# Performance work log

Hardware: AMD Instinct MI355X
Metric: run time of the kernel (lower is better)

Reference implementation:

```python
import jax, jax.numpy as jnp
import numpy as np

N_ROUTES = 512
N_TIMES = 4096
N_MOVES = 16384
N_NODES = 2048
N_CDF = 8192
ALPHA, BETA = 0.15, 4


def setup_inputs() -> dict:
    key = jax.random.key(0)
    ks = jax.random.split(key, 7)
    x_raw = jax.random.normal(ks[0], (N_ROUTES, N_TIMES), dtype=jnp.float32)
    A = (jax.random.uniform(ks[1], (N_MOVES, N_ROUTES)) < 0.05).astype(jnp.float32)
    movement_node = jax.random.randint(ks[2], (N_MOVES,), 0, N_NODES, dtype=jnp.int32)
    cdf_node = jax.random.randint(ks[3], (N_CDF,), 0, N_NODES, dtype=jnp.int32)
    t_free = jax.random.uniform(ks[4], (N_CDF,), minval=0.5, maxval=2.0, dtype=jnp.float32)
    cap = jax.random.uniform(ks[5], (N_CDF,), minval=100.0, maxval=1000.0, dtype=jnp.float32)
    radio = jax.random.uniform(ks[6], (N_CDF,), minval=0.5, maxval=1.5, dtype=jnp.float32)
    return {
        "x_raw": x_raw, "A": A,
        "t_free": t_free, "cap": cap, "radio": radio,
        "movement_node": movement_node, "cdf_node": cdf_node,
        "n_nodes": N_NODES,
    }


def reference(x_raw, A, t_free, cap, radio, movement_node, cdf_node, n_nodes):
    # x = relu(param).clamp(min=0) -> relu is sufficient
    x = jax.nn.relu(x_raw)                                  # [R, T]
    c_pred = A @ x                                          # [M, T]
    # per-node flow: sum of all movement rows sharing the same node
    node_flow = jax.ops.segment_sum(c_pred, movement_node, num_segments=n_nodes)  # [N, T]
    flow = node_flow[cdf_node]                              # [C, T]
    # BPR congestion delay per c_df row
    ratio = jnp.clip(flow / cap[:, None], 1e-6)
    delay_cong = t_free[:, None] * ALPHA * radio[:, None] * ratio ** BETA
    y_rows = t_free[:, None] * radio[:, None] + delay_cong  # [C, T]
    y_l_t_hat = y_rows.sum(axis=0)                          # [T]
    return x, c_pred, y_l_t_hat
```

## Files before the change

### kernel.cpp

```cpp
#include <hip/hip_runtime.h>

#define N_ROUTES 512
#define N_TIMES  4096
#define N_MOVES  16384
#define N_NODES  2048
#define N_CDF    8192
#define ALPHA    0.15f
#define NODE_CAP 32

typedef unsigned short ushort_t;
typedef __attribute__((ext_vector_type(8))) short short8;
typedef __attribute__((ext_vector_type(4))) float floatx4;


__device__ inline ushort_t f2bf(float f) {
    union { float f; unsigned u; } v; v.f = f;
    unsigned r = (v.u + 0x7FFFu + ((v.u >> 16) & 1u)) >> 16;
    return (ushort_t)r;
}

__global__ __launch_bounds__(256) void transpose_bf(const float* __restrict__ xr,
                                                    float* __restrict__ xo,
                                                    ushort_t* __restrict__ xT) {
    __shared__ float ld[64][65];
    int t0 = blockIdx.x * 64;
    int k0 = blockIdx.y * 64;
    int tid = threadIdx.x;
    int col = tid & 63;
    #pragma unroll
    for (int i = 0; i < 16; ++i) {
        int row = i * 4 + (tid >> 6);
        float v = fmaxf(xr[(size_t)(k0 + row) * N_TIMES + t0 + col], 0.f);
        ld[row][col] = v;
        xo[(size_t)(k0 + row) * N_TIMES + t0 + col] = v;
    }
    __syncthreads();
    int trow = tid >> 2;
    int kgrp = (tid & 3) * 16;
    ushort_t __align__(16) tmp[16];
    #pragma unroll
    for (int j = 0; j < 16; ++j) tmp[j] = f2bf(ld[kgrp + j][trow]);
    ushort_t* dst = xT + (size_t)(t0 + trow) * 512 + k0 + kgrp;
    *(uint4*)dst       = ((uint4*)tmp)[0];
    *(uint4*)(dst + 8) = ((uint4*)tmp)[1];
}

__global__ __launch_bounds__(256) void convA(const float* __restrict__ A,
                                             ushort_t* __restrict__ Ab) {
    size_t i = (size_t)(blockIdx.x * 256 + threadIdx.x) * 8;
    const float4* s = (const float4*)(A + i);
    float4 a = s[0], b = s[1];
    ushort_t __align__(16) t[8] = {f2bf(a.x), f2bf(a.y), f2bf(a.z), f2bf(a.w),
                                   f2bf(b.x), f2bf(b.y), f2bf(b.z), f2bf(b.w)};
    *(uint4*)(Ab + i) = *(uint4*)t;
}

__global__ __launch_bounds__(256) void build_nodes(const int* __restrict__ mnode,
                                                   int* __restrict__ ncnt,
                                                   int* __restrict__ nlist) {
    int m = blockIdx.x * blockDim.x + threadIdx.x;
    if (m >= N_MOVES) return;
    int n = mnode[m];
    int slot = atomicAdd(&ncnt[n], 1);
    if (slot < NODE_CAP) nlist[(size_t)n * NODE_CAP + slot] = m;
}

__global__ __launch_bounds__(128) void sa_kernel(const float* __restrict__ A,
                                                 const int* __restrict__ ncnt,
                                                 const int* __restrict__ nlist,
                                                 ushort_t* __restrict__ SAb) {
    int n = blockIdx.x, tid = threadIdx.x;
    int cnt = min(ncnt[n], NODE_CAP);
    float acc0 = 0.f, acc1 = 0.f, acc2 = 0.f, acc3 = 0.f;
    for (int j = 0; j < cnt; ++j) {
        int m = nlist[(size_t)n * NODE_CAP + j];
        float4 v = *(const float4*)(A + (size_t)m * 512 + tid * 4);
        acc0 += v.x; acc1 += v.y; acc2 += v.z; acc3 += v.w;
    }
    ushort_t __align__(8) t[4] = {f2bf(acc0), f2bf(acc1), f2bf(acc2), f2bf(acc3)};
    *(uint2*)(SAb + (size_t)n * 512 + tid * 4) = *(uint2*)t;
}

__global__ __launch_bounds__(256) void wsum_kernel(const float* __restrict__ t_free,
                                                   const float* __restrict__ cap,
                                                   const float* __restrict__ radio,
                                                   const int* __restrict__ cdf_node,
                                                   float* __restrict__ w,
                                                   float* __restrict__ basep) {
    int c = blockIdx.x * 256 + threadIdx.x;
    float tr = t_free[c] * radio[c];
    float ic = 1.0f / cap[c];
    float ic2 = ic * ic;
    atomicAdd(&w[cdf_node[c]], ALPHA * tr * ic2 * ic2);
    float b = tr;
    #pragma unroll
    for (int d = 32; d >= 1; d >>= 1) b += __shfl_down(b, d);
    if ((threadIdx.x & 63) == 0) atomicAdd(basep, b);
}

__global__ __launch_bounds__(256) void y_init(const float* __restrict__ basep,
                                              float* __restrict__ y) {
    y[blockIdx.x * 256 + threadIdx.x] = *basep;
}

#define GLOAD_LDS16(g, l) __builtin_amdgcn_global_load_lds( \
    (const __attribute__((address_space(1))) void*)(g),     \
    (__attribute__((address_space(3))) void*)(l), 16, 0, 0)

__global__ __launch_bounds__(256) void gemm_fused(const ushort_t* __restrict__ Abig,
                                                  const ushort_t* __restrict__ Bbf,
                                                  float* __restrict__ c_pred,
                                                  const float* __restrict__ w,
                                                  float* __restrict__ y) {
    __shared__ __align__(16) ushort_t Atile[2][128 * 64];
    __shared__ __align__(16) ushort_t Btile[2][128 * 64];

    const int tid  = threadIdx.x;
    const int wv   = tid >> 6;
    const int lane = tid & 63;
    const int quad = lane >> 4;
    const int l16  = lane & 15;
    const int bn   = blockIdx.x;
    const int bm   = blockIdx.y;

    const int mi = (wv & 1) * 64;
    const int ni = (wv >> 1) * 64;

    floatx4 acc[4][4] = {};

    const int srow = lane >> 3;
    const int schk = lane & 7;

    const ushort_t* gA = Abig + (size_t)(bm * 128) * 512;
    const ushort_t* gB = Bbf  + (size_t)(bn * 128) * 512;

#define STAGE(buf, kt)                                                       \
    {                                                                        \
        _Pragma("unroll")                                                    \
        for (int c = 0; c < 4; ++c) {                                        \
            int rowbase = wv * 32 + c * 8;                                   \
            int row = rowbase + srow;                                        \
            int cl  = schk ^ (row & 7);                                      \
            GLOAD_LDS16(gA + (size_t)row * 512 + (kt) * 64 + cl * 8,         \
                        &Atile[buf][rowbase * 64]);                          \
            GLOAD_LDS16(gB + (size_t)row * 512 + (kt) * 64 + cl * 8,         \
                        &Btile[buf][rowbase * 64]);                          \
        }                                                                    \
    }

    STAGE(0, 0);
    __syncthreads();

    int cur = 0;
    #pragma unroll
    for (int kt = 0; kt < 8; ++kt) {
        if (kt < 7) STAGE(cur ^ 1, kt + 1);

        #pragma unroll
        for (int kk = 0; kk < 2; ++kk) {
            short8 af[4], bf[4];
            #pragma unroll
            for (int fi = 0; fi < 4; ++fi) {
                int row = mi + fi * 16 + l16;
                int cp  = (kk * 4 + quad) ^ (row & 7);
                af[fi] = *(const short8*)(&Atile[cur][row * 64 + cp * 8]);
            }
            #pragma unroll
            for (int fj = 0; fj < 4; ++fj) {
                int row = ni + fj * 16 + l16;
                int cp  = (kk * 4 + quad) ^ (row & 7);
                bf[fj] = *(const short8*)(&Btile[cur][row * 64 + cp * 8]);
            }
            #pragma unroll
            for (int fi = 0; fi < 4; ++fi)
                #pragma unroll
                for (int fj = 0; fj < 4; ++fj)
                    acc[fi][fj] = __builtin_amdgcn_mfma_f32_16x16x32_bf16(
                        af[fi], bf[fj], acc[fi][fj], 0, 0, 0);
        }

        if (kt < 7) {
            __syncthreads();
            cur ^= 1;
        }
    }
#undef STAGE

    if (bm < 128) {
        #pragma unroll
        for (int fi = 0; fi < 4; ++fi) {
            #pragma unroll
            for (int reg = 0; reg < 4; ++reg) {
                size_t row = (size_t)bm * 128 + mi + fi * 16 + quad * 4 + reg;
                float* cp = c_pred + row * N_TIMES + bn * 128 + ni + l16;
                #pragma unroll
                for (int fj = 0; fj < 4; ++fj)
                    cp[fj * 16] = acc[fi][fj][reg];
            }
        }
    } else {
        int nb = (bm - 128) * 128;
        float psum[4] = {0.f, 0.f, 0.f, 0.f};
        #pragma unroll
        for (int fj = 0; fj < 4; ++fj)
            #pragma unroll
            for (int fi = 0; fi < 4; ++fi)
                #pragma unroll
                for (int reg = 0; reg < 4; ++reg) {
                    int n = nb + mi + fi * 16 + quad * 4 + reg;
                    float f = acc[fi][fj][reg];
                    float f2 = f * f;
                    psum[fj] += w[n] * f2 * f2;
                }
        #pragma unroll
        for (int fj = 0; fj < 4; ++fj) {
            float v = psum[fj];
            v += __shfl_xor(v, 16);
            v += __shfl_xor(v, 32);
            if (quad == 0)
                atomicAdd(&y[bn * 128 + ni + fj * 16 + l16], v);
        }
    }
}

extern "C" void kernel_launch(void* const* d_in, const int* in_sizes, int n_in,
                              void* d_out, int out_size, void* d_ws, size_t ws_size,
                              hipStream_t stream) {
    const float* x_raw         = (const float*)d_in[0];
    const float* A             = (const float*)d_in[1];
    const float* t_free        = (const float*)d_in[2];
    const float* cap           = (const float*)d_in[3];
    const float* radio         = (const float*)d_in[4];
    const int*   movement_node = (const int*)d_in[5];
    const int*   cdf_node      = (const int*)d_in[6];

    float* out    = (float*)d_out;
    float* x_out  = out;
    float* c_pred = out + (size_t)N_ROUTES * N_TIMES;
    float* y      = c_pred + (size_t)N_MOVES * N_TIMES;

    char* ws = (char*)d_ws;
    ushort_t* Abig  = (ushort_t*)(ws);
    ushort_t* SAb   = Abig + (size_t)N_MOVES * 512;
    ushort_t* xTbf  = (ushort_t*)(ws + 18874368);
    int*      ncnt  = (int*)(ws + 23068672);
    int*      nlist = (int*)(ws + 23076864);
    float*    w     = (float*)(ws + 23339008);
    float*    basep = (float*)(ws + 23347200);

    hipMemsetAsync(ncnt, 0, N_NODES * sizeof(int), stream);
    hipMemsetAsync(w, 0, N_NODES * sizeof(float), stream);
    hipMemsetAsync(basep, 0, sizeof(float), stream);

    transpose_bf<<<dim3(N_TIMES / 64, N_ROUTES / 64), dim3(256), 0, stream>>>(
        x_raw, x_out, xTbf);

    convA<<<dim3((int)((size_t)N_MOVES * 512 / 8 / 256)), dim3(256), 0, stream>>>(A, Abig);

    build_nodes<<<dim3(N_MOVES / 256), dim3(256), 0, stream>>>(movement_node, ncnt, nlist);

    sa_kernel<<<dim3(N_NODES), dim3(128), 0, stream>>>(A, ncnt, nlist, SAb);

    wsum_kernel<<<dim3(N_CDF / 256), dim3(256), 0, stream>>>(
        t_free, cap, radio, cdf_node, w, basep);

    y_init<<<dim3(N_TIMES / 256), dim3(256), 0, stream>>>(basep, y);

    gemm_fused<<<dim3(N_TIMES / 128, (N_MOVES + N_NODES) / 128), dim3(256), 0, stream>>>(
        Abig, xTbf, c_pred, w, y);
}
```

Before: 412.9 us.

## Restructure fused GEMM into 256x256 tiles with 8-wave ping-pong pipeline

Moves the fused GEMM from 128x128 tiles and 4 waves to 256x256 tiles and 8 waves. It splits each K-step into quadrant MFMA phases that interleave LDS reads, async global-to-LDS loads with explicit vmcnt waits and raw s_barrier, and uses s_setprio around the MFMA bursts. A 1D grid with an XCD-aware swizzle replaces the 2D grid. The goal is more data reuse per tile and better overlap of memory with matrix cores. The cost is higher register and LDS pressure (128KB LDS per block) and hand-tuned barrier ordering that is fragile.

```diff
diff --git a/kernel.cpp b/kernel.cpp
--- a/kernel.cpp
+++ b/kernel.cpp
@@ -107,107 +107,153 @@
     (const __attribute__((address_space(1))) void*)(g),     \
     (__attribute__((address_space(3))) void*)(l), 16, 0, 0)
 
-__global__ __launch_bounds__(256) void gemm_fused(const ushort_t* __restrict__ Abig,
-                                                  const ushort_t* __restrict__ Bbf,
-                                                  float* __restrict__ c_pred,
-                                                  const float* __restrict__ w,
-                                                  float* __restrict__ y) {
-    __shared__ __align__(16) ushort_t Atile[2][128 * 64];
-    __shared__ __align__(16) ushort_t Btile[2][128 * 64];
+__global__ __launch_bounds__(512, 2) void gemm_fused(const ushort_t* __restrict__ Abig,
+                                                     const ushort_t* __restrict__ Bbf,
+                                                     float* __restrict__ c_pred,
+                                                     const float* __restrict__ w,
+                                                     float* __restrict__ y) {
+    __shared__ __align__(16) ushort_t lds[4][256 * 64];
 
     const int tid  = threadIdx.x;
     const int wv   = tid >> 6;
     const int lane = tid & 63;
     const int quad = lane >> 4;
     const int l16  = lane & 15;
-    const int bn   = blockIdx.x;
-    const int bm   = blockIdx.y;
-
-    const int mi = (wv & 1) * 64;
-    const int ni = (wv >> 1) * 64;
-
-    floatx4 acc[4][4] = {};
-
-    const int srow = lane >> 3;
-    const int schk = lane & 7;
-
-    const ushort_t* gA = Abig + (size_t)(bm * 128) * 512;
-    const ushort_t* gB = Bbf  + (size_t)(bn * 128) * 512;
-
-#define STAGE(buf, kt)                                                       \
-    {                                                                        \
-        _Pragma("unroll")                                                    \
-        for (int c = 0; c < 4; ++c) {                                        \
-            int rowbase = wv * 32 + c * 8;                                   \
-            int row = rowbase + srow;                                        \
-            int cl  = schk ^ (row & 7);                                      \
-            GLOAD_LDS16(gA + (size_t)row * 512 + (kt) * 64 + cl * 8,         \
-                        &Atile[buf][rowbase * 64]);                          \
-            GLOAD_LDS16(gB + (size_t)row * 512 + (kt) * 64 + cl * 8,         \
-                        &Btile[buf][rowbase * 64]);                          \
-        }                                                                    \
+    const int wr   = wv >> 2;
+    const int wc   = wv & 3;
+
+    const int bid = blockIdx.x;
+    const int swz = (bid & 7) * 144 + (bid >> 3);
+    const int bm  = swz >> 4;
+    const int bn  = swz & 15;
+
+    ushort_t* AE = &lds[0][0];
+    ushort_t* AO = &lds[1][0];
+    ushort_t* BE = &lds[2][0];
+    ushort_t* BO = &lds[3][0];
+
+    const ushort_t* gA = Abig + (size_t)bm * 256 * 512;
+    const ushort_t* gB = Bbf  + (size_t)bn * 256 * 512;
+
+    const int rr = wv * 8 + (lane >> 3);
+    const int cl = (lane & 7) ^ (lane >> 3);
+
+#define STAGE_HALF(T, G, r0, kt) do {                                          \
+        GLOAD_LDS16((G) + (size_t)((r0) + rr) * 512 + (kt) * 64 + cl * 8,      \
+                    (T) + ((r0) + wv * 8) * 64);                               \
+        GLOAD_LDS16((G) + (size_t)((r0) + 64 + rr) * 512 + (kt) * 64 + cl * 8, \
+                    (T) + ((r0) + 64 + wv * 8) * 64);                          \
+    } while (0)
+
+#define BAR()  asm volatile("s_barrier" ::: "memory")
+#define VMC4() asm volatile("s_waitcnt vmcnt(4)" ::: "memory")
+
+    short8 af[4][2];
+    short8 b0[2][2];
+    short8 b1[2][2];
+    floatx4 acc[8][4] = {};
+
+#define READ_A(T, qm) do {                                                     \
+        _Pragma("unroll")                                                      \
+        for (int fi = 0; fi < 4; ++fi) {                                       \
+            int row = wr * 128 + (qm) * 64 + fi * 16 + l16;                    \
+            const ushort_t* p = (T) + row * 64;                                \
+            af[fi][0] = *(const short8*)(p + ((quad       ^ (l16 & 7)) * 8));  \
+            af[fi][1] = *(const short8*)(p + (((4 + quad) ^ (l16 & 7)) * 8));  \
+        }                                                                      \
+    } while (0)
+
+#define READ_B(T, qn, B) do {                                                  \
+        _Pragma("unroll")                                                      \
+        for (int fj = 0; fj < 2; ++fj) {                                       \
+            int row = wc * 64 + (qn) * 32 + fj * 16 + l16;                     \
+            const ushort_t* p = (T) + row * 64;                                \
+            B[fj][0] = *(const short8*)(p + ((quad       ^ (l16 & 7)) * 8));   \
+            B[fj][1] = *(const short8*)(p + (((4 + quad) ^ (l16 & 7)) * 8));   \
+        }                                                                      \
+    } while (0)
+
+#define MFMA_Q(qm, qn, B) do {                                                 \
+        __builtin_amdgcn_s_setprio(1);                                         \
+        _Pragma("unroll")                                                      \
+        for (int kk = 0; kk < 2; ++kk)                                         \
+            _Pragma("unroll")                                                  \
+            for (int fi = 0; fi < 4; ++fi)                                     \
+                _Pragma("unroll")                                              \
+                for (int fj = 0; fj < 2; ++fj)                                 \
+                    acc[(qm) * 4 + fi][(qn) * 2 + fj] =                        \
+                        __builtin_amdgcn_mfma_f32_16x16x32_bf16(               \
+                            af[fi][kk], B[fj][kk],                             \
+                            acc[(qm) * 4 + fi][(qn) * 2 + fj], 0, 0, 0);       \
+        __builtin_amdgcn_s_setprio(0);                                         \
+    } while (0)
+
+    STAGE_HALF(AE, gA, 0, 0);   STAGE_HALF(AE, gA, 128, 0);
+    STAGE_HALF(BE, gB, 0, 0);   STAGE_HALF(BE, gB, 128, 0);
+    STAGE_HALF(BO, gB, 0, 1);   STAGE_HALF(BO, gB, 128, 1);
+    VMC4();
+    BAR();
+
+    for (int t = 0; t < 4; ++t) {
+        const int o  = 2 * t + 1;
+        const int e2 = 2 * t + 2;
+        const int o2 = 2 * t + 3;
+
+        READ_A(AE, 0); READ_B(BE, 0, b0);
+        STAGE_HALF(AO, gA, 0, o);
+        BAR(); MFMA_Q(0, 0, b0); BAR();
+        READ_B(BE, 1, b1);
+        STAGE_HALF(AO, gA, 128, o);
+        BAR(); MFMA_Q(0, 1, b1); BAR();
+        READ_A(AE, 1);
+        STAGE_HALF(BE, gB, 0, e2);
+        BAR(); MFMA_Q(1, 0, b0); BAR();
+        STAGE_HALF(BE, gB, 128, e2);
+        VMC4();
+        BAR(); MFMA_Q(1, 1, b1); BAR();
+        READ_A(AO, 0); READ_B(BO, 0, b0);
+        STAGE_HALF(AE, gA, 0, e2);
+        BAR(); MFMA_Q(0, 0, b0); BAR();
+        READ_B(BO, 1, b1);
+        STAGE_HALF(AE, gA, 128, e2);
+        BAR(); MFMA_Q(0, 1, b1); BAR();
+        READ_A(AO, 1);
+        STAGE_HALF(BO, gB, 0, o2);
+        BAR(); MFMA_Q(1, 0, b0); BAR();
+        STAGE_HALF(BO, gB, 128, o2);
+        VMC4();
+        BAR(); MFMA_Q(1, 1, b1); BAR();
     }
 
-    STAGE(0, 0);
-    __syncthreads();
-
-    int cur = 0;
-    #pragma unroll
-    for (int kt = 0; kt < 8; ++kt) {
-        if (kt < 7) STAGE(cur ^ 1, kt + 1);
-
+#undef STAGE_HALF
+#undef READ_A
+#undef READ_B
+#undef MFMA_Q
+#undef BAR
+#undef VMC4
+
+    if (bm < 64) {
         #pragma unroll
-        for (int kk = 0; kk < 2; ++kk) {
-            short8 af[4], bf[4];
-            #pragma unroll
-            for (int fi = 0; fi < 4; ++fi) {
-                int row = mi + fi * 16 + l16;
-                int cp  = (kk * 4 + quad) ^ (row & 7);
-                af[fi] = *(const short8*)(&Atile[cur][row * 64 + cp * 8]);
-            }
-            #pragma unroll
-            for (int fj = 0; fj < 4; ++fj) {
-                int row = ni + fj * 16 + l16;
-                int cp  = (kk * 4 + quad) ^ (row & 7);
-                bf[fj] = *(const short8*)(&Btile[cur][row * 64 + cp * 8]);
-            }
-            #pragma unroll
-            for (int fi = 0; fi < 4; ++fi)
-                #pragma unroll
-                for (int fj = 0; fj < 4; ++fj)
-                    acc[fi][fj] = __builtin_amdgcn_mfma_f32_16x16x32_bf16(
-                        af[fi], bf[fj], acc[fi][fj], 0, 0, 0);
-        }
-
-        if (kt < 7) {
-            __syncthreads();
-            cur ^= 1;
-        }
-    }
-#undef STAGE
-
-    if (bm < 128) {
-        #pragma unroll
-        for (int fi = 0; fi < 4; ++fi) {
+        for (int fi = 0; fi < 8; ++fi) {
             #pragma unroll
             for (int reg = 0; reg < 4; ++reg) {
-                size_t row = (size_t)bm * 128 + mi + fi * 16 + quad * 4 + reg;
-                float* cp = c_pred + row * N_TIMES + bn * 128 + ni + l16;
+                size_t row = (size_t)bm * 256 + wr * 128 + fi * 16 + quad * 4 + reg;
+                float* cp = c_pred + row * N_TIMES + bn * 256 + wc * 64 + l16;
                 #pragma unroll
                 for (int fj = 0; fj < 4; ++fj)
                     cp[fj * 16] = acc[fi][fj][reg];
             }
         }
     } else {
-        int nb = (bm - 128) * 128;
+        int nb = (bm - 64) * 256 + wr * 128;
         float psum[4] = {0.f, 0.f, 0.f, 0.f};
         #pragma unroll
         for (int fj = 0; fj < 4; ++fj)
             #pragma unroll
-            for (int fi = 0; fi < 4; ++fi)
+            for (int fi = 0; fi < 8; ++fi)
                 #pragma unroll
                 for (int reg = 0; reg < 4; ++reg) {
-                    int n = nb + mi + fi * 16 + quad * 4 + reg;
+                    int n = nb + fi * 16 + quad * 4 + reg;
                     float f = acc[fi][fj][reg];
                     float f2 = f * f;
                     psum[fj] += w[n] * f2 * f2;
@@ -218,7 +264,7 @@
             v += __shfl_xor(v, 16);
             v += __shfl_xor(v, 32);
             if (quad == 0)
-                atomicAdd(&y[bn * 128 + ni + fj * 16 + l16], v);
+                atomicAdd(&y[bn * 256 + wc * 64 + fj * 16 + l16], v);
         }
     }
 }
@@ -266,6 +312,6 @@
 
     y_init<<<dim3(N_TIMES / 256), dim3(256), 0, stream>>>(basep, y);
 
-    gemm_fused<<<dim3(N_TIMES / 128, (N_MOVES + N_NODES) / 128), dim3(256), 0, stream>>>(
+    gemm_fused<<<dim3((N_TIMES / 256) * ((N_MOVES + N_NODES) / 256)), dim3(512), 0, stream>>>(
         Abig, xTbf, c_pred, w, y);
 }
```

Result: no change. 405.4 us (-1.8%).
